# Performance work log

Hardware: AMD Instinct MI355X
Metric: run time of the kernel (lower is better)

## Reference

```python
import jax, jax.numpy as jnp
import numpy as np

HEADS = 16
HEAD_DIM = 32
WINDOW = 64  # kernel_size = 2*WINDOW + 1 = 129
NEG = -1e30


def setup_inputs() -> dict:
    key = jax.random.key(0)
    ks = jax.random.split(key, 9)
    B, T, D, G = 4, 8192, HEADS * HEAD_DIM, 64
    x = jax.random.normal(ks[0], (B, T, D), jnp.float32)
    def W(k):
        return jax.random.normal(k, (D, D), jnp.float32) * 0.02
    def b(k):
        return jax.random.normal(k, (D,), jnp.float32) * 0.02
    return {
        "x": x,
        "Wq": W(ks[1]), "bq": b(ks[2]),
        "Wk": W(ks[3]), "bk": b(ks[4]),
        "Wv": W(ks[5]), "bv": b(ks[6]),
        "Wo": W(ks[7]), "bo": b(ks[8]),
        "global_idx": jnp.arange(G, dtype=jnp.int64 if jax.config.jax_enable_x64 else jnp.int32),
    }


def _sparse_global_attn(x, Wq, bq, Wk, bk, Wv, bv, Wo, bo, global_idx):
    B, T, D = x.shape
    H, d, w = HEADS, HEAD_DIM, WINDOW
    scale = 1.0 / (d ** 0.5)

    def proj(W, b):
        # (B,T,D) -> (B,H,T,d)
        return (x @ W + b).reshape(B, T, H, d).transpose(0, 2, 1, 3)

    q, k, v = proj(Wq, bq), proj(Wk, bk), proj(Wv, bv)

    offsets = jnp.arange(-w, w + 1)  # (K,)
    K = offsets.shape[0]

    # Local band scores: score[b,h,t,j] = <q[t], k[t+offset_j]>, computed
    # offset-by-offset via roll to avoid a (B,H,T,K,d) gather.
    def score_step(_, o):
        s = jnp.einsum('bhtd,bhtd->bht', q, jnp.roll(k, -o, axis=2))
        return None, s
    _, loc = jax.lax.scan(score_step, None, offsets)  # (K,B,H,T)
    loc = jnp.moveaxis(loc, 0, -1) * scale            # (B,H,T,K)

    pos = jnp.arange(T)[:, None] + offsets[None, :]   # (T,K)
    valid = (pos >= 0) & (pos < T)
    loc = jnp.where(valid[None, None], loc, NEG)

    # Global-token scores (global tokens shared across the batch)
    k_g = k[:, :, global_idx, :]                      # (B,H,G,d)
    v_g = v[:, :, global_idx, :]
    gsc = jnp.einsum('bhtd,bhgd->bhtg', q, k_g) * scale  # (B,H,T,G)

    # Joint softmax over [local window | global tokens] (duplicates where a
    # global token lies inside the local window, matching the original).
    attn = jax.nn.softmax(jnp.concatenate([loc, gsc], axis=-1), axis=-1)
    a_loc = jnp.moveaxis(attn[..., :K], -1, 0)        # (K,B,H,T)
    a_g = attn[..., K:]                               # (B,H,T,G)

    def ctx_step(acc, oa):
        o, a = oa
        return acc + a[..., None] * jnp.roll(v, -o, axis=2), None
    ctx, _ = jax.lax.scan(ctx_step, jnp.zeros_like(q), (offsets, a_loc))
    ctx = ctx + jnp.einsum('bhtg,bhgd->bhtd', a_g, v_g)  # (B,H,T,d)

    out = ctx.transpose(0, 2, 1, 3).reshape(B, T, D)
    return out @ Wo + bo


def reference(x, Wq, bq, Wk, bk, Wv, bv, Wo, bo, global_idx):
    return _sparse_global_attn(x, Wq, bq, Wk, bk, Wv, bv, Wo, bo, global_idx)
```

## Files before the change

kernel.cpp:

```cpp
#include <hip/hip_runtime.h>
#include <hip/hip_bf16.h>
#include <cstdint>
#include <cstddef>

using bf16 = __hip_bfloat16;
typedef __bf16 bf16x8 __attribute__((ext_vector_type(8)));
typedef __bf16 bf16x4 __attribute__((ext_vector_type(4)));
typedef float f32x4 __attribute__((ext_vector_type(4)));

constexpr int BB = 4;
constexpr int TS = 8192;
constexpr int NH = 16;
constexpr int HD = 32;
constexpr int DM = 512;
constexpr int NQKV = 1536;
constexpr int NG = 64;

#define MFMA16(a, b, c) __builtin_amdgcn_mfma_f32_16x16x32_bf16((a), (b), (c), 0, 0, 0)

__device__ __forceinline__ bf16x8 ld8(const bf16* p) { return *(const bf16x8*)p; }
__device__ __forceinline__ bf16x4 ld4(const bf16* p) { return *(const bf16x4*)p; }
__device__ __forceinline__ unsigned short b16bits(bf16 v) { return __builtin_bit_cast(unsigned short, v); }

__device__ __forceinline__ void gl_lds16(const bf16* g, void* l) {
  __builtin_amdgcn_global_load_lds((const __attribute__((address_space(1))) void*)g,
                                   (__attribute__((address_space(3))) void*)l, 16, 0, 0);
}

__global__ void prep_kernel(const float* __restrict__ x,
                            const float* __restrict__ Wq, const float* __restrict__ bq,
                            const float* __restrict__ Wk, const float* __restrict__ bk,
                            const float* __restrict__ Wv, const float* __restrict__ bv,
                            const float* __restrict__ Wo,
                            bf16* __restrict__ xb, bf16* __restrict__ Wt,
                            bf16* __restrict__ Wot, float* __restrict__ bqkv) {
  const int64_t stride = (int64_t)gridDim.x * blockDim.x;
  const int64_t i0 = (int64_t)blockIdx.x * blockDim.x + threadIdx.x;
  const float4* x4 = (const float4*)x;
  ushort4* xb4 = (ushort4*)xb;
  for (int64_t i = i0; i < (int64_t)BB * TS * DM / 4; i += stride) {
    float4 v = x4[i];
    ushort4 o;
    o.x = b16bits(__float2bfloat16(v.x));
    o.y = b16bits(__float2bfloat16(v.y));
    o.z = b16bits(__float2bfloat16(v.z));
    o.w = b16bits(__float2bfloat16(v.w));
    xb4[i] = o;
  }
  for (int64_t i = i0; i < (int64_t)NQKV * DM; i += stride) {
    const int n = (int)(i >> 9), k = (int)(i & 511);
    const float* W = (n < 512) ? Wq : ((n < 1024) ? Wk : Wv);
    Wt[i] = __float2bfloat16(W[(size_t)k * DM + (n & 511)]);
  }
  for (int64_t i = i0; i < (int64_t)DM * DM; i += stride) {
    const int n = (int)(i >> 9), k = (int)(i & 511);
    Wot[i] = __float2bfloat16(Wo[(size_t)k * DM + n]);
  }
  for (int64_t i = i0; i < NQKV; i += stride)
    bqkv[i] = (i < 512) ? bq[i] : ((i < 1024) ? bk[i - 512] : bv[i - 1024]);
}

template <bool F32OUT, bool WVT>
__global__ __launch_bounds__(256) void gemm_bias(const bf16* __restrict__ A,
                                                 const bf16* __restrict__ Bt,
                                                 const float* __restrict__ bias,
                                                 void* __restrict__ Cv,
                                                 bf16* __restrict__ vt,
                                                 int M, int N, int K, int cpx) {
  __shared__ __attribute__((aligned(16))) char smem[65536];
  const int tid = threadIdx.x;
  const int lane = tid & 63, wid = tid >> 6;
  const int grp = lane >> 4, col = lane & 15;
  const int bid = (blockIdx.x & 7) * cpx + (blockIdx.x >> 3);
  const int NT = N >> 7;
  const int mt = bid / NT, nt = bid % NT;
  const int m0 = mt << 7, n0 = nt << 7;
  const int wm = wid >> 1, wn = wid & 1;
  f32x4 acc[4][4] = {};
  const int KT = K >> 6;

  auto stage = [&](int kt, int d) {
    #pragma unroll
    for (int c = 0; c < 4; ++c) {
      const int chunk = wid * 4 + c;
      const int row = chunk * 8 + (lane >> 3);
      const int sl = lane & 7;
      const int koff = ((sl ^ (row & 7)) << 3) + (kt << 6);
      gl_lds16(A + (size_t)(m0 + row) * K + koff, smem + d * 16384 + chunk * 1024);
      gl_lds16(Bt + (size_t)(n0 + row) * K + koff,
               smem + 32768 + d * 16384 + chunk * 1024);
    }
  };

  stage(0, 0);
  for (int kt = 0; kt < KT; ++kt) {
    const int cur = kt & 1;
    if (kt + 1 < KT) {
      stage(kt + 1, cur ^ 1);
      __builtin_amdgcn_sched_barrier(0);
      asm volatile("s_waitcnt vmcnt(8)" ::: "memory");
    } else {
      __builtin_amdgcn_sched_barrier(0);
      asm volatile("s_waitcnt vmcnt(0)" ::: "memory");
    }
    __builtin_amdgcn_sched_barrier(0);
    __builtin_amdgcn_s_barrier();
    __builtin_amdgcn_sched_barrier(0);
    const char* sA = smem + cur * 16384;
    const char* sB = smem + 32768 + cur * 16384;
    #pragma unroll
    for (int ks = 0; ks < 2; ++ks) {
      bf16x8 af[4], bfr[4];
      #pragma unroll
      for (int f = 0; f < 4; ++f) {
        const int ra = wm * 64 + f * 16 + col;
        af[f] = *(const bf16x8*)(sA + ra * 128 + (((ks * 4 + grp) ^ (ra & 7)) << 4));
        const int rb = wn * 64 + f * 16 + col;
        bfr[f] = *(const bf16x8*)(sB + rb * 128 + (((ks * 4 + grp) ^ (rb & 7)) << 4));
      }
      #pragma unroll
      for (int i = 0; i < 4; ++i)
        #pragma unroll
        for (int j = 0; j < 4; ++j)
          acc[i][j] = MFMA16(af[i], bfr[j], acc[i][j]);
    }
    __builtin_amdgcn_sched_barrier(0);
    __builtin_amdgcn_s_barrier();
    __builtin_amdgcn_sched_barrier(0);
  }
  const bool wv = WVT && (n0 >= 1024);
  if (!wv) {
    #pragma unroll
    for (int i = 0; i < 4; ++i)
      #pragma unroll
      for (int j = 0; j < 4; ++j) {
        const int n = n0 + wn * 64 + j * 16 + col;
        const float bz = bias[n];
        #pragma unroll
        for (int r = 0; r < 4; ++r) {
          const int m = m0 + wm * 64 + i * 16 + grp * 4 + r;
          const float v = acc[i][j][r] + bz;
          if (F32OUT)
            ((float*)Cv)[(size_t)m * N + n] = v;
          else
            ((bf16*)Cv)[(size_t)m * N + n] = __float2bfloat16(v);
        }
      }
  } else {
    __syncthreads();
    bf16* lt = (bf16*)smem;
    #pragma unroll
    for (int i = 0; i < 4; ++i)
      #pragma unroll
      for (int j = 0; j < 4; ++j) {
        const int nl = wn * 64 + j * 16 + col;
        const float bz = bias[n0 + nl];
        #pragma unroll
        for (int r = 0; r < 4; ++r) {
          const int ml = wm * 64 + i * 16 + grp * 4 + r;
          lt[nl * 136 + (ml ^ ((nl & 7) << 4))] = __float2bfloat16(acc[i][j][r] + bz);
        }
      }
    __syncthreads();
    const int row = tid >> 1, half = tid & 1;
    const int b = m0 >> 13, t0 = m0 & 8191;
    bf16* dst = vt + (size_t)(b * DM + (n0 & 511) + row) * TS + t0 + half * 64;
    const bf16* srcl = lt + row * 136;
    #pragma unroll
    for (int c = 0; c < 8; ++c)
      *(bf16x8*)(dst + c * 8) =
          *(const bf16x8*)(srcl + ((half * 64 + c * 8) ^ ((row & 7) << 4)));
  }
}

__global__ void vgt_kernel(const bf16* __restrict__ vt, const int* __restrict__ gidx,
                           bf16* __restrict__ vtp, bf16* __restrict__ vgt) {
  const int64_t stride = (int64_t)gridDim.x * blockDim.x;
  const int64_t i0 = (int64_t)blockIdx.x * blockDim.x + threadIdx.x;
  for (int64_t i = i0; i < 512; i += stride) {
    if (i < 64) vtp[i - 64] = __float2bfloat16(0.f);
    else vtp[(size_t)2048 * TS + (i - 64)] = __float2bfloat16(0.f);
  }
  for (int64_t i = i0; i < (int64_t)2048 * NG; i += stride) {
    const int row = (int)(i >> 6), g = (int)(i & 63);
    const int gi = gidx[g];
    vgt[i] = vt[(size_t)row * TS + gi];
  }
}

__global__ __launch_bounds__(256) void attn_kernel(const bf16* __restrict__ qkv,
                                                   const bf16* __restrict__ vt,
                                                   const bf16* __restrict__ vgt,
                                                   const int* __restrict__ gidx,
                                                   bf16* __restrict__ ctx) {
  constexpr int VST = 216;
  constexpr int VGST = 88;
  __shared__ __attribute__((aligned(16))) char smem[35840];
  bf16* sV = (bf16*)smem;
  bf16* sVg = (bf16*)(smem + 13824);
  bf16* sK = (bf16*)(smem + 19456);
  bf16* sKg = (bf16*)(smem + 31744);

  const int tid = threadIdx.x, wid = tid >> 6, lane = tid & 63;
  const int grp = lane >> 4, col = lane & 15;
  const int bid = (blockIdx.x & 7) * 1024 + (blockIdx.x >> 3);
  const int tile = bid & 127, h = (bid >> 7) & 15, b = bid >> 11;
  const int t0b = tile * 64;
  const int kbb = t0b - 64;
  const int bh = b * NH + h;
  const bf16* base = qkv + (size_t)b * TS * NQKV;
  const bf16* kpl = base + 512 + h * 32;

  #pragma unroll
  for (int it = 0; it < 3; ++it) {
    const int idx = it * 256 + tid;
    const int row = idx >> 2, part = idx & 3;
    const int tok = min(max(kbb + row, 0), TS - 1);
    gl_lds16(kpl + (size_t)tok * NQKV + ((part ^ (row & 3)) << 3), sK + idx * 8);
  }
  {
    const int row = tid >> 2, part = tid & 3;
    const int gi = gidx[row];
    gl_lds16(kpl + (size_t)gi * NQKV + ((part ^ (row & 3)) << 3), sKg + tid * 8);
  }
  {
    const bf16* vr = vt + (size_t)(bh * HD + (tid >> 3)) * TS + kbb;
    #pragma unroll
    for (int i = 0; i < 4; ++i) {
      const int c = i * 8 + (tid & 7);
      if (c < 27) *(bf16x8*)(sV + (tid >> 3) * VST + c * 8) = ld8(vr + c * 8);
    }
  }
  {
    const int row = tid >> 3, c = tid & 7;
    *(bf16x8*)(sVg + row * VGST + c * 8) = ld8(vgt + (size_t)(bh * HD + row) * NG + c * 8);
  }
  __syncthreads();

  const int qt = t0b + wid * 16;
  const int offw = wid * 16;

  const bf16x8 qf = ld8(base + (size_t)(qt + col) * NQKV + h * 32 + grp * 8);
  const f32x4 z = {0.f, 0.f, 0.f, 0.f};
  f32x4 s[13];
  #pragma unroll
  for (int f = 0; f < 9; ++f) {
    const int row = offw + f * 16 + col;
    bf16x8 kf = ld8(sK + row * 32 + ((grp ^ (row & 3)) << 3));
    s[f] = MFMA16(kf, qf, z);
  }
  #pragma unroll
  for (int f = 0; f < 4; ++f) {
    const int row = f * 16 + col;
    bf16x8 kf = ld8(sKg + row * 32 + ((grp ^ (row & 3)) << 3));
    s[9 + f] = MFMA16(kf, qf, z);
  }
  const float scale = 0.17677669529663688f;
  float mx = -3e38f;
  const bool interior = (tile >= 1) & (tile <= 126);
  if (interior) {
    #pragma unroll
    for (int f = 0; f < 13; ++f) {
      #pragma unroll
      for (int r = 0; r < 4; ++r) {
        float v = s[f][r] * scale;
        if (f == 0) v = (grp * 4 + r >= col) ? v : -1e30f;
        if (f == 8) v = (grp * 4 + r <= col) ? v : -1e30f;
        s[f][r] = v;
        mx = fmaxf(mx, v);
      }
    }
  } else {
    #pragma unroll
    for (int f = 0; f < 13; ++f) {
      #pragma unroll
      for (int r = 0; r < 4; ++r) {
        float v = s[f][r] * scale;
        if (f < 9) {
          const int j = f * 16 + grp * 4 + r;
          const int pos = qt - 64 + j;
          const bool valid = (j >= col) & (j <= col + 128) & (pos >= 0) & (pos < TS);
          v = valid ? v : -1e30f;
        }
        s[f][r] = v;
        mx = fmaxf(mx, v);
      }
    }
  }
  mx = fmaxf(mx, __shfl_xor(mx, 16));
  mx = fmaxf(mx, __shfl_xor(mx, 32));
  float sum = 0.f;
  bf16x8 pb[7];
  #pragma unroll
  for (int f = 0; f < 13; ++f) {
    const int pr = (f < 9) ? (f >> 1) : (5 + ((f - 9) >> 1));
    const int hf = (f < 9) ? (f & 1) : ((f - 9) & 1);
    #pragma unroll
    for (int r = 0; r < 4; ++r) {
      float p = __expf(s[f][r] - mx);
      sum += p;
      pb[pr][hf * 4 + r] = (__bf16)__float2bfloat16(p);
    }
  }
  #pragma unroll
  for (int r = 0; r < 4; ++r) pb[4][4 + r] = (__bf16)__float2bfloat16(0.f);
  sum += __shfl_xor(sum, 16);
  sum += __shfl_xor(sum, 32);
  const float sm = 1.0f / sum;

  f32x4 c0 = z, c1 = z;
  const bf16* sVr0 = sV + col * VST;
  const bf16* sVr1 = sV + (col + 16) * VST;
  #pragma unroll
  for (int i = 0; i < 5; ++i) {
    const int kk = offw + i * 32 + grp * 4;
    bf16x8 a0 = __builtin_shufflevector(ld4(sVr0 + kk), ld4(sVr0 + kk + 16),
                                        0, 1, 2, 3, 4, 5, 6, 7);
    bf16x8 a1 = __builtin_shufflevector(ld4(sVr1 + kk), ld4(sVr1 + kk + 16),
                                        0, 1, 2, 3, 4, 5, 6, 7);
    c0 = MFMA16(a0, pb[i], c0);
    c1 = MFMA16(a1, pb[i], c1);
  }
  const bf16* sVg0 = sVg + col * VGST;
  const bf16* sVg1 = sVg + (col + 16) * VGST;
  #pragma unroll
  for (int i = 0; i < 2; ++i) {
    const int kk = i * 32 + grp * 4;
    bf16x8 a0 = __builtin_shufflevector(ld4(sVg0 + kk), ld4(sVg0 + kk + 16),
                                        0, 1, 2, 3, 4, 5, 6, 7);
    bf16x8 a1 = __builtin_shufflevector(ld4(sVg1 + kk), ld4(sVg1 + kk + 16),
                                        0, 1, 2, 3, 4, 5, 6, 7);
    c0 = MFMA16(a0, pb[5 + i], c0);
    c1 = MFMA16(a1, pb[5 + i], c1);
  }
  const int t = qt + col;
  bf16* op = ctx + ((size_t)(b * TS + t)) * DM + h * 32 + grp * 4;
  ushort4 o0, o1;
  o0.x = b16bits(__float2bfloat16(c0[0] * sm));
  o0.y = b16bits(__float2bfloat16(c0[1] * sm));
  o0.z = b16bits(__float2bfloat16(c0[2] * sm));
  o0.w = b16bits(__float2bfloat16(c0[3] * sm));
  o1.x = b16bits(__float2bfloat16(c1[0] * sm));
  o1.y = b16bits(__float2bfloat16(c1[1] * sm));
  o1.z = b16bits(__float2bfloat16(c1[2] * sm));
  o1.w = b16bits(__float2bfloat16(c1[3] * sm));
  *(ushort4*)op = o0;
  *(ushort4*)(op + 16) = o1;
}

extern "C" void kernel_launch(void* const* d_in, const int* in_sizes, int n_in,
                              void* d_out, int out_size, void* d_ws, size_t ws_size,
                              hipStream_t stream) {
  (void)in_sizes; (void)n_in; (void)out_size; (void)ws_size;
  const float* x = (const float*)d_in[0];
  const float* Wq = (const float*)d_in[1];
  const float* bq = (const float*)d_in[2];
  const float* Wk = (const float*)d_in[3];
  const float* bk = (const float*)d_in[4];
  const float* Wv = (const float*)d_in[5];
  const float* bv = (const float*)d_in[6];
  const float* Wo = (const float*)d_in[7];
  const float* bo = (const float*)d_in[8];
  const int* gidx = (const int*)d_in[9];
  float* out = (float*)d_out;

  char* ws = (char*)d_ws;
  size_t off = 0;
  auto alloc = [&](size_t bytes) -> void* {
    void* p = ws + off;
    off += (bytes + 255) & ~(size_t)255;
    return p;
  };
  bf16* xb = (bf16*)alloc((size_t)BB * TS * DM * 2);
  bf16* Wt = (bf16*)alloc((size_t)NQKV * DM * 2);
  bf16* Wot = (bf16*)alloc((size_t)DM * DM * 2);
  float* bqkv = (float*)alloc((size_t)NQKV * 4);
  bf16* qkv = (bf16*)alloc((size_t)BB * TS * NQKV * 2);
  bf16* vta = (bf16*)alloc(((size_t)2048 * TS + 512) * 2);
  bf16* vgt = (bf16*)alloc((size_t)2048 * NG * 2);
  bf16* ctx = xb;
  bf16* vt = vta + 64;

  prep_kernel<<<dim3(2048), dim3(256), 0, stream>>>(x, Wq, bq, Wk, bk, Wv, bv, Wo,
                                                    xb, Wt, Wot, bqkv);
  gemm_bias<false, true><<<dim3(3072), dim3(256), 0, stream>>>(xb, Wt, bqkv, qkv, vt,
                                                               BB * TS, NQKV, DM, 384);
  vgt_kernel<<<dim3(512), dim3(256), 0, stream>>>(vt, gidx, vt, vgt);
  attn_kernel<<<dim3(8192), dim3(256), 0, stream>>>(qkv, vt, vgt, gidx, ctx);
  gemm_bias<true, false><<<dim3(1024), dim3(256), 0, stream>>>(ctx, Wot, bo, out, nullptr,
                                                               BB * TS, DM, DM, 128);
}
```

Baseline: 172.8 us.

## Enlarge GEMM tiles to 256x128 with 512 threads and triple-buffered LDS pipeline

The projection GEMMs now use 8 waves per block computing a 256x128 output tile instead of 128x128. Loads are issued two k-steps ahead into a three-stage LDS ring, with adjusted vmcnt waits. Fragments for both k-substeps are preloaded before the MFMAs, which are wrapped in s_setprio. The intent is to deepen latency hiding and improve B-tile reuse, at the cost of 144KB LDS per block (one block per CU) and fewer blocks in the grid.

```diff
diff --git a/kernel.cpp b/kernel.cpp
--- a/kernel.cpp
+++ b/kernel.cpp
@@ -61,68 +61,74 @@
 }
 
 template <bool F32OUT, bool WVT>
-__global__ __launch_bounds__(256) void gemm_bias(const bf16* __restrict__ A,
+__global__ __launch_bounds__(512) void gemm_bias(const bf16* __restrict__ A,
                                                  const bf16* __restrict__ Bt,
                                                  const float* __restrict__ bias,
                                                  void* __restrict__ Cv,
                                                  bf16* __restrict__ vt,
                                                  int M, int N, int K, int cpx) {
-  __shared__ __attribute__((aligned(16))) char smem[65536];
+  __shared__ __attribute__((aligned(16))) char smem[147456];
   const int tid = threadIdx.x;
   const int lane = tid & 63, wid = tid >> 6;
   const int grp = lane >> 4, col = lane & 15;
   const int bid = (blockIdx.x & 7) * cpx + (blockIdx.x >> 3);
   const int NT = N >> 7;
   const int mt = bid / NT, nt = bid % NT;
-  const int m0 = mt << 7, n0 = nt << 7;
+  const int m0 = mt << 8, n0 = nt << 7;
   const int wm = wid >> 1, wn = wid & 1;
   f32x4 acc[4][4] = {};
   const int KT = K >> 6;
 
-  auto stage = [&](int kt, int d) {
+  auto stage = [&](int kt) {
+    char* buf = smem + (kt % 3) * 49152;
     #pragma unroll
     for (int c = 0; c < 4; ++c) {
-      const int chunk = wid * 4 + c;
-      const int row = chunk * 8 + (lane >> 3);
-      const int sl = lane & 7;
+      const int idx = c * 512 + tid;
+      const int row = idx >> 3, sl = idx & 7;
       const int koff = ((sl ^ (row & 7)) << 3) + (kt << 6);
-      gl_lds16(A + (size_t)(m0 + row) * K + koff, smem + d * 16384 + chunk * 1024);
-      gl_lds16(Bt + (size_t)(n0 + row) * K + koff,
-               smem + 32768 + d * 16384 + chunk * 1024);
+      gl_lds16(A + (size_t)(m0 + row) * K + koff, buf + idx * 16);
+    }
+    #pragma unroll
+    for (int c = 0; c < 2; ++c) {
+      const int idx = c * 512 + tid;
+      const int row = idx >> 3, sl = idx & 7;
+      const int koff = ((sl ^ (row & 7)) << 3) + (kt << 6);
+      gl_lds16(Bt + (size_t)(n0 + row) * K + koff, buf + 32768 + idx * 16);
     }
   };
 
-  stage(0, 0);
+  stage(0);
+  stage(1);
   for (int kt = 0; kt < KT; ++kt) {
-    const int cur = kt & 1;
-    if (kt + 1 < KT) {
-      stage(kt + 1, cur ^ 1);
-      __builtin_amdgcn_sched_barrier(0);
-      asm volatile("s_waitcnt vmcnt(8)" ::: "memory");
-    } else {
-      __builtin_amdgcn_sched_barrier(0);
-      asm volatile("s_waitcnt vmcnt(0)" ::: "memory");
-    }
+    if (kt + 2 < KT) stage(kt + 2);
+    __builtin_amdgcn_sched_barrier(0);
+    if (kt + 2 < KT)      asm volatile("s_waitcnt vmcnt(12)" ::: "memory");
+    else if (kt + 1 < KT) asm volatile("s_waitcnt vmcnt(6)" ::: "memory");
+    else                  asm volatile("s_waitcnt vmcnt(0)" ::: "memory");
     __builtin_amdgcn_sched_barrier(0);
     __builtin_amdgcn_s_barrier();
     __builtin_amdgcn_sched_barrier(0);
-    const char* sA = smem + cur * 16384;
-    const char* sB = smem + 32768 + cur * 16384;
-    #pragma unroll
-    for (int ks = 0; ks < 2; ++ks) {
-      bf16x8 af[4], bfr[4];
+    const char* sA = smem + (kt % 3) * 49152;
+    const char* sB = sA + 32768;
+    bf16x8 af[2][4], bfr[2][4];
+    #pragma unroll
+    for (int ks = 0; ks < 2; ++ks)
       #pragma unroll
       for (int f = 0; f < 4; ++f) {
         const int ra = wm * 64 + f * 16 + col;
-        af[f] = *(const bf16x8*)(sA + ra * 128 + (((ks * 4 + grp) ^ (ra & 7)) << 4));
+        af[ks][f] = *(const bf16x8*)(sA + ra * 128 + (((ks * 4 + grp) ^ (ra & 7)) << 4));
         const int rb = wn * 64 + f * 16 + col;
-        bfr[f] = *(const bf16x8*)(sB + rb * 128 + (((ks * 4 + grp) ^ (rb & 7)) << 4));
-      }
+        bfr[ks][f] = *(const bf16x8*)(sB + rb * 128 + (((ks * 4 + grp) ^ (rb & 7)) << 4));
+      }
+    #pragma unroll
+    for (int ks = 0; ks < 2; ++ks) {
+      __builtin_amdgcn_s_setprio(1);
       #pragma unroll
       for (int i = 0; i < 4; ++i)
         #pragma unroll
         for (int j = 0; j < 4; ++j)
-          acc[i][j] = MFMA16(af[i], bfr[j], acc[i][j]);
+          acc[i][j] = MFMA16(af[ks][i], bfr[ks][j], acc[i][j]);
+      __builtin_amdgcn_s_setprio(0);
     }
     __builtin_amdgcn_sched_barrier(0);
     __builtin_amdgcn_s_barrier();
@@ -158,18 +164,18 @@
         #pragma unroll
         for (int r = 0; r < 4; ++r) {
           const int ml = wm * 64 + i * 16 + grp * 4 + r;
-          lt[nl * 136 + (ml ^ ((nl & 7) << 4))] = __float2bfloat16(acc[i][j][r] + bz);
+          lt[nl * 264 + (ml ^ ((nl & 7) << 4))] = __float2bfloat16(acc[i][j][r] + bz);
         }
       }
     __syncthreads();
-    const int row = tid >> 1, half = tid & 1;
+    const int row = tid >> 2, q = tid & 3;
     const int b = m0 >> 13, t0 = m0 & 8191;
-    bf16* dst = vt + (size_t)(b * DM + (n0 & 511) + row) * TS + t0 + half * 64;
-    const bf16* srcl = lt + row * 136;
+    bf16* dst = vt + (size_t)(b * DM + (n0 & 511) + row) * TS + t0 + q * 64;
+    const bf16* srcl = lt + row * 264;
     #pragma unroll
     for (int c = 0; c < 8; ++c)
       *(bf16x8*)(dst + c * 8) =
-          *(const bf16x8*)(srcl + ((half * 64 + c * 8) ^ ((row & 7) << 4)));
+          *(const bf16x8*)(srcl + ((q * 64 + c * 8) ^ ((row & 7) << 4)));
   }
 }
 
@@ -383,10 +389,10 @@
 
   prep_kernel<<<dim3(2048), dim3(256), 0, stream>>>(x, Wq, bq, Wk, bk, Wv, bv, Wo,
                                                     xb, Wt, Wot, bqkv);
-  gemm_bias<false, true><<<dim3(3072), dim3(256), 0, stream>>>(xb, Wt, bqkv, qkv, vt,
-                                                               BB * TS, NQKV, DM, 384);
+  gemm_bias<false, true><<<dim3(1536), dim3(512), 0, stream>>>(xb, Wt, bqkv, qkv, vt,
+                                                               BB * TS, NQKV, DM, 192);
   vgt_kernel<<<dim3(512), dim3(256), 0, stream>>>(vt, gidx, vt, vgt);
   attn_kernel<<<dim3(8192), dim3(256), 0, stream>>>(qkv, vt, vgt, gidx, ctx);
-  gemm_bias<true, false><<<dim3(1024), dim3(256), 0, stream>>>(ctx, Wot, bo, out, nullptr,
-                                                               BB * TS, DM, DM, 128);
-}
+  gemm_bias<true, false><<<dim3(512), dim3(512), 0, stream>>>(ctx, Wot, bo, out, nullptr,
+                                                              BB * TS, DM, DM, 64);
+}
```

New measurement: 186.9 us. 1.08x slower.

## Pre-pack weights in MFMA fragment order and load B operand straight to registers

Applied to the files above, without the earlier changes.

The prep kernel now writes the QKV and output weights in the exact per-lane MFMA fragment order. The GEMM can then load its B operand directly from global memory into registers, with one 16-byte load per fragment, instead of staging it through LDS. Shared memory drops from 64KB to about 34KB and launch bounds ask for 3 blocks per SM, which targets higher occupancy and less LDS traffic. The trade-offs are more register pressure from the prefetched B fragments, a strided gather in the prep kernel, and B loads that may no longer be coalesced across waves.

```diff
diff --git a/kernel.cpp b/kernel.cpp
--- a/kernel.cpp
+++ b/kernel.cpp
@@ -32,8 +32,8 @@
                             const float* __restrict__ Wk, const float* __restrict__ bk,
                             const float* __restrict__ Wv, const float* __restrict__ bv,
                             const float* __restrict__ Wo,
-                            bf16* __restrict__ xb, bf16* __restrict__ Wt,
-                            bf16* __restrict__ Wot, float* __restrict__ bqkv) {
+                            bf16* __restrict__ xb, bf16* __restrict__ Wp,
+                            bf16* __restrict__ Wp2, float* __restrict__ bqkv) {
   const int64_t stride = (int64_t)gridDim.x * blockDim.x;
   const int64_t i0 = (int64_t)blockIdx.x * blockDim.x + threadIdx.x;
   const float4* x4 = (const float4*)x;
@@ -47,27 +47,38 @@
     o.w = b16bits(__float2bfloat16(v.w));
     xb4[i] = o;
   }
-  for (int64_t i = i0; i < (int64_t)NQKV * DM; i += stride) {
-    const int n = (int)(i >> 9), k = (int)(i & 511);
+  for (int64_t c = i0; c < (int64_t)NQKV * DM / 8; c += stride) {
+    const int lane = (int)(c & 63), f = (int)((c >> 6) & 3), ks = (int)((c >> 8) & 1);
+    const int kt = (int)((c >> 9) & 7), wn = (int)((c >> 12) & 1), nt = (int)(c >> 13);
+    const int n = nt * 128 + wn * 64 + f * 16 + (lane & 15);
+    const int k = kt * 64 + ks * 32 + (lane >> 4) * 8;
     const float* W = (n < 512) ? Wq : ((n < 1024) ? Wk : Wv);
-    Wt[i] = __float2bfloat16(W[(size_t)k * DM + (n & 511)]);
-  }
-  for (int64_t i = i0; i < (int64_t)DM * DM; i += stride) {
-    const int n = (int)(i >> 9), k = (int)(i & 511);
-    Wot[i] = __float2bfloat16(Wo[(size_t)k * DM + n]);
+    const int nn = n & 511;
+    #pragma unroll
+    for (int j = 0; j < 8; ++j)
+      Wp[c * 8 + j] = __float2bfloat16(W[(size_t)(k + j) * DM + nn]);
+  }
+  for (int64_t c = i0; c < (int64_t)DM * DM / 8; c += stride) {
+    const int lane = (int)(c & 63), f = (int)((c >> 6) & 3), ks = (int)((c >> 8) & 1);
+    const int kt = (int)((c >> 9) & 7), wn = (int)((c >> 12) & 1), nt = (int)(c >> 13);
+    const int n = nt * 128 + wn * 64 + f * 16 + (lane & 15);
+    const int k = kt * 64 + ks * 32 + (lane >> 4) * 8;
+    #pragma unroll
+    for (int j = 0; j < 8; ++j)
+      Wp2[c * 8 + j] = __float2bfloat16(Wo[(size_t)(k + j) * DM + n]);
   }
   for (int64_t i = i0; i < NQKV; i += stride)
     bqkv[i] = (i < 512) ? bq[i] : ((i < 1024) ? bk[i - 512] : bv[i - 1024]);
 }
 
 template <bool F32OUT, bool WVT>
-__global__ __launch_bounds__(256) void gemm_bias(const bf16* __restrict__ A,
-                                                 const bf16* __restrict__ Bt,
-                                                 const float* __restrict__ bias,
-                                                 void* __restrict__ Cv,
-                                                 bf16* __restrict__ vt,
-                                                 int M, int N, int K, int cpx) {
-  __shared__ __attribute__((aligned(16))) char smem[65536];
+__global__ __launch_bounds__(256, 3) void gemm_bias(const bf16* __restrict__ A,
+                                                    const bf16* __restrict__ Bp,
+                                                    const float* __restrict__ bias,
+                                                    void* __restrict__ Cv,
+                                                    bf16* __restrict__ vt,
+                                                    int M, int N, int K, int cpx) {
+  __shared__ __attribute__((aligned(16))) char smem[35072];
   const int tid = threadIdx.x;
   const int lane = tid & 63, wid = tid >> 6;
   const int grp = lane >> 4, col = lane & 15;
@@ -76,29 +87,37 @@
   const int mt = bid / NT, nt = bid % NT;
   const int m0 = mt << 7, n0 = nt << 7;
   const int wm = wid >> 1, wn = wid & 1;
+  const int KT = K >> 6;
   f32x4 acc[4][4] = {};
-  const int KT = K >> 6;
-
-  auto stage = [&](int kt, int d) {
+
+  const bf16* bp = Bp + (size_t)(nt * 2 + wn) * KT * 4096 + lane * 8;
+  bf16x8 breg[2][4];
+  auto loadB = [&](int kt) {
+    #pragma unroll
+    for (int ks = 0; ks < 2; ++ks)
+      #pragma unroll
+      for (int f = 0; f < 4; ++f)
+        breg[ks][f] = ld8(bp + (size_t)(kt * 8 + ks * 4 + f) * 512);
+  };
+  auto stageA = [&](int kt) {
+    char* buf = smem + (kt & 1) * 16384;
     #pragma unroll
     for (int c = 0; c < 4; ++c) {
       const int chunk = wid * 4 + c;
       const int row = chunk * 8 + (lane >> 3);
       const int sl = lane & 7;
       const int koff = ((sl ^ (row & 7)) << 3) + (kt << 6);
-      gl_lds16(A + (size_t)(m0 + row) * K + koff, smem + d * 16384 + chunk * 1024);
-      gl_lds16(Bt + (size_t)(n0 + row) * K + koff,
-               smem + 32768 + d * 16384 + chunk * 1024);
+      gl_lds16(A + (size_t)(m0 + row) * K + koff, buf + chunk * 1024);
     }
   };
 
-  stage(0, 0);
+  stageA(0);
+  loadB(0);
   for (int kt = 0; kt < KT; ++kt) {
-    const int cur = kt & 1;
     if (kt + 1 < KT) {
-      stage(kt + 1, cur ^ 1);
+      stageA(kt + 1);
       __builtin_amdgcn_sched_barrier(0);
-      asm volatile("s_waitcnt vmcnt(8)" ::: "memory");
+      asm volatile("s_waitcnt vmcnt(4)" ::: "memory");
     } else {
       __builtin_amdgcn_sched_barrier(0);
       asm volatile("s_waitcnt vmcnt(0)" ::: "memory");
@@ -106,28 +125,27 @@
     __builtin_amdgcn_sched_barrier(0);
     __builtin_amdgcn_s_barrier();
     __builtin_amdgcn_sched_barrier(0);
-    const char* sA = smem + cur * 16384;
-    const char* sB = smem + 32768 + cur * 16384;
+    const char* sA = smem + (kt & 1) * 16384;
     #pragma unroll
     for (int ks = 0; ks < 2; ++ks) {
-      bf16x8 af[4], bfr[4];
+      bf16x8 af[4];
       #pragma unroll
       for (int f = 0; f < 4; ++f) {
         const int ra = wm * 64 + f * 16 + col;
         af[f] = *(const bf16x8*)(sA + ra * 128 + (((ks * 4 + grp) ^ (ra & 7)) << 4));
-        const int rb = wn * 64 + f * 16 + col;
-        bfr[f] = *(const bf16x8*)(sB + rb * 128 + (((ks * 4 + grp) ^ (rb & 7)) << 4));
       }
       #pragma unroll
       for (int i = 0; i < 4; ++i)
         #pragma unroll
         for (int j = 0; j < 4; ++j)
-          acc[i][j] = MFMA16(af[i], bfr[j], acc[i][j]);
-    }
+          acc[i][j] = MFMA16(af[i], breg[ks][j], acc[i][j]);
+    }
+    if (kt + 1 < KT) loadB(kt + 1);
     __builtin_amdgcn_sched_barrier(0);
     __builtin_amdgcn_s_barrier();
     __builtin_amdgcn_sched_barrier(0);
   }
+
   const bool wv = WVT && (n0 >= 1024);
   if (!wv) {
     #pragma unroll
@@ -372,8 +390,8 @@
     return p;
   };
   bf16* xb = (bf16*)alloc((size_t)BB * TS * DM * 2);
-  bf16* Wt = (bf16*)alloc((size_t)NQKV * DM * 2);
-  bf16* Wot = (bf16*)alloc((size_t)DM * DM * 2);
+  bf16* Wp = (bf16*)alloc((size_t)NQKV * DM * 2);
+  bf16* Wp2 = (bf16*)alloc((size_t)DM * DM * 2);
   float* bqkv = (float*)alloc((size_t)NQKV * 4);
   bf16* qkv = (bf16*)alloc((size_t)BB * TS * NQKV * 2);
   bf16* vta = (bf16*)alloc(((size_t)2048 * TS + 512) * 2);
@@ -382,11 +400,11 @@
   bf16* vt = vta + 64;
 
   prep_kernel<<<dim3(2048), dim3(256), 0, stream>>>(x, Wq, bq, Wk, bk, Wv, bv, Wo,
-                                                    xb, Wt, Wot, bqkv);
-  gemm_bias<false, true><<<dim3(3072), dim3(256), 0, stream>>>(xb, Wt, bqkv, qkv, vt,
+                                                    xb, Wp, Wp2, bqkv);
+  gemm_bias<false, true><<<dim3(3072), dim3(256), 0, stream>>>(xb, Wp, bqkv, qkv, vt,
                                                                BB * TS, NQKV, DM, 384);
   vgt_kernel<<<dim3(512), dim3(256), 0, stream>>>(vt, gidx, vt, vgt);
   attn_kernel<<<dim3(8192), dim3(256), 0, stream>>>(qkv, vt, vgt, gidx, ctx);
-  gemm_bias<true, false><<<dim3(1024), dim3(256), 0, stream>>>(ctx, Wot, bo, out, nullptr,
+  gemm_bias<true, false><<<dim3(1024), dim3(256), 0, stream>>>(ctx, Wp2, bo, out, nullptr,
                                                                BB * TS, DM, DM, 128);
 }
```

Result: faster. 168.0 us (-2.8%).
